# Performance work log

Measured on AMD Instinct MI355X. Metric: run time of the kernel, lower is better.

Reference implementation:

```python
import jax, jax.numpy as jnp
import numpy as np

B, C, H, W = 8, 512, 64, 64
CDIV = 8
CFG = C // CDIV  # f/g channels = 64


def setup_inputs() -> dict:
    key = jax.random.key(0)
    ks = jax.random.split(key, 8)
    x = jax.random.normal(ks[0], (B, C, H, W), dtype=jnp.float32)
    # 1x1 conv weights (spectral-norm omitted: weights used as-given), orthogonal-ish small init
    Wf = jax.random.normal(ks[1], (CFG, C), dtype=jnp.float32) * 0.02
    bf = jnp.zeros((CFG,), dtype=jnp.float32)
    Wg = jax.random.normal(ks[2], (CFG, C), dtype=jnp.float32) * 0.02
    bg = jnp.zeros((CFG,), dtype=jnp.float32)
    Wh = jax.random.normal(ks[3], (C, C), dtype=jnp.float32) * 0.02
    bh = jnp.zeros((C,), dtype=jnp.float32)
    # module inits gamma=0 (identity output); use 0.5 so the attention path is exercised
    gamma = jnp.float32(0.5)
    return {"x": x, "Wf": Wf, "bf": bf, "Wg": Wg, "bg": bg, "Wh": Wh, "bh": bh, "gamma": gamma}


def reference(x, Wf, bf, Wg, bg, Wh, bh, gamma):
    Bb, Cc, Hh, Ww = x.shape
    N = Hh * Ww
    xf = x.reshape(Bb, Cc, N)  # [B, C, N]
    # 1x1 convs == per-pixel linear maps
    f = jnp.einsum('oc,bcn->bon', Wf, xf) + bf[:, None]  # [B, CFG, N]
    g = jnp.einsum('oc,bcn->bon', Wg, xf) + bg[:, None]  # [B, CFG, N]
    h = jnp.einsum('oc,bcn->bon', Wh, xf) + bh[:, None]  # [B, C, N]
    # attention scores over spatial tokens: queries g, keys f -> [B, N, N]
    s = jnp.einsum('bci,bcj->bij', g, f)
    beta = jax.nn.softmax(s, axis=-1)
    o = jnp.einsum('bij,bcj->bci', beta, h).reshape(Bb, Cc, Hh, Ww)
    return gamma * o + x
```

## Files before the change

kernel.cpp:

```cpp
#include <hip/hip_runtime.h>
#include <hip/hip_bf16.h>

typedef __bf16 bf16;
typedef __attribute__((ext_vector_type(2))) __bf16 bf16x2;
typedef __attribute__((ext_vector_type(4))) __bf16 bf16x4;
typedef __attribute__((ext_vector_type(8))) __bf16 bf16x8;
typedef __attribute__((ext_vector_type(4))) float f32x4;
typedef __attribute__((ext_vector_type(4))) int i32x4;
typedef __attribute__((ext_vector_type(8))) int i32x8;
typedef unsigned char u8;

#define MFMA16x16x32 __builtin_amdgcn_mfma_f32_16x16x32_bf16
#define MFMA_MX(a, b, c, sa, sb) \
    __builtin_amdgcn_mfma_scale_f32_16x16x128_f8f6f4((a), (b), (c), 0, 0, 0, (sa), 0, (sb))

#define CAT8(lo, hi) (i32x8){(lo)[0], (lo)[1], (lo)[2], (lo)[3], (hi)[0], (hi)[1], (hi)[2], (hi)[3]}

#define NB 8
#define NC 512
#define NN 4096
#define CFG 64

#define XP 520
#define TP 74

#define EXP_OFF 4.5f
#define SCALE_ONE 0x7F7F7F7F

__global__ __launch_bounds__(256) void k_wprep(
    const float* __restrict__ Wf, const float* __restrict__ bfv,
    const float* __restrict__ Wg, const float* __restrict__ bgv,
    const float* __restrict__ Wh,
    bf16* __restrict__ Wfg, bf16* __restrict__ Whb, float* __restrict__ bfg)
{
    int idx = blockIdx.x * 256 + threadIdx.x;
    if (idx < 32768)       Wfg[idx] = (bf16)Wf[idx];
    else if (idx < 65536)  Wfg[idx] = (bf16)Wg[idx - 32768];
    if (idx < 262144)      Whb[idx] = (bf16)Wh[idx];
    if (idx < 64)          bfg[idx] = bfv[idx];
    else if (idx < 128)    bfg[idx] = bgv[idx - 64];
}

__global__ __launch_bounds__(512) void k_fused(
    const float* __restrict__ x, const bf16* __restrict__ Wfg,
    const float* __restrict__ bfg, const bf16* __restrict__ Whb,
    const float* __restrict__ bh,
    bf16* __restrict__ fF, bf16* __restrict__ gF, u8* __restrict__ hT)
{
    __shared__ bf16 X[64 * XP];
    __shared__ bf16 tile[64 * TP];

    int b = blockIdx.x, n0 = blockIdx.y * 64;
    int t = threadIdx.x;

    for (int cc = 0; cc < 8; cc++) {
        int cl = t >> 3, seg = (t & 7) * 8;
        const float* src = x + ((size_t)(b * NC + cc * 64 + cl)) * NN + n0 + seg;
        float4 v0 = ((const float4*)src)[0];
        float4 v1 = ((const float4*)src)[1];
        bf16* tr = &tile[cl * TP + seg];
        *(bf16x2*)(tr + 0) = bf16x2{(bf16)v0.x, (bf16)v0.y};
        *(bf16x2*)(tr + 2) = bf16x2{(bf16)v0.z, (bf16)v0.w};
        *(bf16x2*)(tr + 4) = bf16x2{(bf16)v1.x, (bf16)v1.y};
        *(bf16x2*)(tr + 6) = bf16x2{(bf16)v1.z, (bf16)v1.w};
        __syncthreads();
        int nl = t >> 3, cs = (t & 7) * 8;
        bf16 buf[8];
#pragma unroll
        for (int u = 0; u < 8; u++) buf[u] = tile[(cs + u) * TP + nl];
        *(bf16x8*)&X[nl * XP + cc * 64 + cs] = *(bf16x8*)buf;
        __syncthreads();
    }

    int w = t >> 6, l = t & 63;
    int lr = l & 15, lq = l >> 4;

    {
        const bf16* Ab = Whb + (size_t)(w * 64) * NC;
        f32x4 acc[4][4] = {};
        for (int k0 = 0; k0 < NC; k0 += 32) {
            bf16x8 a[4], bb[4];
#pragma unroll
            for (int fi = 0; fi < 4; fi++)
                a[fi] = *(const bf16x8*)(Ab + (size_t)(fi*16 + lr) * NC + k0 + lq*8);
#pragma unroll
            for (int fj = 0; fj < 4; fj++)
                bb[fj] = *(const bf16x8*)&X[(fj*16 + lr) * XP + k0 + lq*8];
#pragma unroll
            for (int fi = 0; fi < 4; fi++)
#pragma unroll
                for (int fj = 0; fj < 4; fj++)
                    acc[fi][fj] = MFMA16x16x32(bb[fj], a[fi], acc[fi][fj], 0, 0, 0);
        }
#pragma unroll
        for (int fi = 0; fi < 4; fi++) {
            int c = w*64 + fi*16 + lr;
            float bias = bh[c];
            size_t ctile = (size_t)(c >> 4);
#pragma unroll
            for (int fj = 0; fj < 4; fj++) {
                int j0 = n0 + fj*16 + lq*4;
                float v0 = acc[fi][fj][0] + bias;
                float v1 = acc[fi][fj][1] + bias;
                float v2 = acc[fi][fj][2] + bias;
                float v3 = acc[fi][fj][3] + bias;
                int pk = __builtin_amdgcn_cvt_pk_fp8_f32(v0, v1, 0, false);
                pk     = __builtin_amdgcn_cvt_pk_fp8_f32(v2, v3, pk, true);
                size_t tile128 = (size_t)(b*32) + (size_t)(j0 >> 7);
                size_t hk   = (size_t)((j0 >> 4) & 1);
                size_t lane = (size_t)(((j0 >> 5) & 3)*16 + (c & 15));
                size_t off = ((tile128*32 + ctile)*2 + hk)*1024 + lane*16 + (size_t)(j0 & 15);
                *(int*)(hT + off) = pk;
            }
        }
    }

    {
        const bf16* Bb = Wfg + (size_t)(w * 16) * NC;
        f32x4 acc2[4] = {};
        for (int k0 = 0; k0 < NC; k0 += 32) {
            bf16x8 a[4], bo;
#pragma unroll
            for (int fi = 0; fi < 4; fi++)
                a[fi] = *(const bf16x8*)&X[(fi*16 + lr) * XP + k0 + lq*8];
            bo = *(const bf16x8*)(Bb + (size_t)lr * NC + k0 + lq*8);
#pragma unroll
            for (int fi = 0; fi < 4; fi++)
                acc2[fi] = MFMA16x16x32(a[fi], bo, acc2[fi], 0, 0, 0);
        }
#pragma unroll
        for (int fi = 0; fi < 4; fi++)
#pragma unroll
            for (int tt = 0; tt < 4; tt++) {
                int n = n0 + fi*16 + lq*4 + tt;
                int o = w*16 + lr;
                float v = acc2[fi][tt] + bfg[o];
                int c = o & 63;
                bf16* dst = (o < 64) ? fF : gF;
                int jt16 = n >> 4, nr = n & 15;
                int ks = c >> 5, lqd = (c >> 3) & 3, e = c & 7;
                size_t off = (((size_t)(b*256 + jt16)*2 + ks)*64 + (lqd*16 + nr))*8 + e;
                dst[off] = (bf16)v;
            }
    }
}

__global__ __launch_bounds__(1024, 4) void k_attn(
    const bf16* __restrict__ fF, const bf16* __restrict__ gF,
    const u8* __restrict__ hT, const float* __restrict__ x,
    const float* __restrict__ gammap, float* __restrict__ out)
{
    __shared__ alignas(16) u8 Pl[2][16384];
    __shared__ alignas(16) bf16 fS[2][8192];
    __shared__ float lpart[8][2][16];
    __shared__ alignas(16) float linv[128];

    int b  = blockIdx.x;
    int i0 = blockIdx.y * 128;
    int t = threadIdx.x;
    int w = t >> 6, l = t & 63;
    int lr = l & 15, lq = l >> 4;

    float gamma = *gammap;
    int fi_s = w >> 1;
    int ks_s = w & 1;
    const int sone = SCALE_ONE;

    u8* Pf = &Pl[0][0];

    const bf16* gbase = gF + ((size_t)(b*256 + (i0 >> 4) + fi_s)*2)*512 + (size_t)l*8;
    bf16x8 bg0 = *(const bf16x8*)(gbase);
    bf16x8 bg1 = *(const bf16x8*)(gbase + 512);

    const bf16* fb0 = fF + (size_t)b*256*2*512;
    const u8* hb0 = hT + (size_t)b*2097152 + (size_t)(w*2)*2048 + (size_t)l*16;

    f32x4 oacc[8][2] = {};
    float lsum = 0.f;

#define F_LOAD(q, reg)  { (reg) = *(const bf16x8*)(fb0 + (size_t)(q)*8192 + t*8); }
#define F_WRITE(q, reg) { *(bf16x8*)&fS[(q) & 1][t*8] = (reg); }

#define S_STEP(jn, fbuf, pbuf)                                                 \
    {                                                                          \
        const bf16* fb = &fS[fbuf][((jn) & 1)*4096 + ks_s*2048] + l*8;         \
        bf16x8 af00 = *(const bf16x8*)(fb);                                    \
        bf16x8 af01 = *(const bf16x8*)(fb + 512);                              \
        bf16x8 af10 = *(const bf16x8*)(fb + 1024);                             \
        bf16x8 af11 = *(const bf16x8*)(fb + 1536);                             \
        f32x4 s0 = {}, s1 = {};                                                \
        s0 = MFMA16x16x32(af00, bg0, s0, 0, 0, 0);                             \
        s0 = MFMA16x16x32(af01, bg1, s0, 0, 0, 0);                             \
        s1 = MFMA16x16x32(af10, bg0, s1, 0, 0, 0);                             \
        s1 = MFMA16x16x32(af11, bg1, s1, 0, 0, 0);                             \
        float e00 = __expf(s0[0] - EXP_OFF), e01 = __expf(s0[1] - EXP_OFF);    \
        float e02 = __expf(s0[2] - EXP_OFF), e03 = __expf(s0[3] - EXP_OFF);    \
        float e10 = __expf(s1[0] - EXP_OFF), e11 = __expf(s1[1] - EXP_OFF);    \
        float e12 = __expf(s1[2] - EXP_OFF), e13 = __expf(s1[3] - EXP_OFF);    \
        lsum += (e00 + e01 + e02 + e03) + (e10 + e11 + e12 + e13);             \
        int pk0 = __builtin_amdgcn_cvt_pk_fp8_f32(e00, e01, 0, false);         \
        pk0     = __builtin_amdgcn_cvt_pk_fp8_f32(e02, e03, pk0, true);        \
        int pk1 = __builtin_amdgcn_cvt_pk_fp8_f32(e10, e11, 0, false);         \
        pk1     = __builtin_amdgcn_cvt_pk_fp8_f32(e12, e13, pk1, true);        \
        u8* pw = Pf + (pbuf)*16384 + fi_s*2048                                 \
                 + ((((jn) & 1)*2 + ks_s)*16 + lr)*16 + lq*4;                  \
        *(int*)(pw)        = pk0;                                              \
        *(int*)(pw + 1024) = pk1;                                              \
    }

#define PV_STEP(ph, pbuf)                                                      \
    {                                                                          \
        const u8* hb = hb0 + (size_t)(ph)*65536;                               \
        i32x4 hl0 = *(const i32x4*)(hb);                                       \
        i32x4 hh0 = *(const i32x4*)(hb + 1024);                                \
        i32x4 hl1 = *(const i32x4*)(hb + 2048);                                \
        i32x4 hh1 = *(const i32x4*)(hb + 3072);                                \
        i32x8 ah0 = CAT8(hl0, hh0);                                            \
        i32x8 ah1 = CAT8(hl1, hh1);                                            \
        const u8* Pr = Pf + (pbuf)*16384 + l*16;                               \
        __builtin_amdgcn_s_setprio(1);                                         \
        _Pragma("unroll")                                                      \
        for (int fi = 0; fi < 8; fi++) {                                       \
            i32x4 plo = *(const i32x4*)(Pr + fi*2048);                         \
            i32x4 phi = *(const i32x4*)(Pr + fi*2048 + 1024);                  \
            i32x8 ap = CAT8(plo, phi);                                         \
            oacc[fi][0] = MFMA_MX(ap, ah0, oacc[fi][0], sone, sone);           \
            oacc[fi][1] = MFMA_MX(ap, ah1, oacc[fi][1], sone, sone);           \
        }                                                                      \
        __builtin_amdgcn_s_setprio(0);                                         \
    }

    {
        bf16x8 fr;
        F_LOAD(0, fr)
        F_WRITE(0, fr)
        __syncthreads();
        F_LOAD(1, fr)
        S_STEP(0, 0, 0)
        S_STEP(1, 0, 0)
        F_WRITE(1, fr)
        __syncthreads();
    }

    for (int p = 0; p < 30; p++) {
        int cur = p & 1, nxt = cur ^ 1;

        bf16x8 fr;
        F_LOAD(p + 2, fr)

        PV_STEP(p, cur)

        S_STEP(2*p + 2, nxt, nxt)
        S_STEP(2*p + 3, nxt, nxt)

        F_WRITE(p + 2, fr)

        __syncthreads();
    }

    PV_STEP(30, 0)
    S_STEP(62, 1, 1)
    S_STEP(63, 1, 1)
    __syncthreads();
    PV_STEP(31, 1)

#undef S_STEP
#undef PV_STEP
#undef F_LOAD
#undef F_WRITE

    lsum += __shfl_xor(lsum, 16, 64);
    lsum += __shfl_xor(lsum, 32, 64);
    if (lq == 0) lpart[fi_s][ks_s][lr] = lsum;
    __syncthreads();
    if (t < 128) {
        linv[t] = 1.0f / (lpart[t >> 4][0][t & 15] + lpart[t >> 4][1][t & 15]);
    }
    __syncthreads();

    int cw = w * 32;
    const float* xb = x + (size_t)b * NC * NN;
    float* ob = out + (size_t)b * NC * NN;
#pragma unroll
    for (int fi = 0; fi < 8; fi++) {
        f32x4 li = *(const f32x4*)&linv[fi*16 + lq*4];
#pragma unroll
        for (int fc = 0; fc < 2; fc++) {
            int c = cw + fc*16 + lr;
            size_t base = (size_t)c * NN + i0 + fi*16 + lq*4;
            float4 xv = *(const float4*)(xb + base);
            float4 ov;
            ov.x = gamma * oacc[fi][fc][0] * li[0] + xv.x;
            ov.y = gamma * oacc[fi][fc][1] * li[1] + xv.y;
            ov.z = gamma * oacc[fi][fc][2] * li[2] + xv.z;
            ov.w = gamma * oacc[fi][fc][3] * li[3] + xv.w;
            *(float4*)(ob + base) = ov;
        }
    }
}

extern "C" void kernel_launch(void* const* d_in, const int* in_sizes, int n_in,
                              void* d_out, int out_size, void* d_ws, size_t ws_size,
                              hipStream_t stream)
{
    const float* x     = (const float*)d_in[0];
    const float* Wf    = (const float*)d_in[1];
    const float* bf_   = (const float*)d_in[2];
    const float* Wg    = (const float*)d_in[3];
    const float* bg_   = (const float*)d_in[4];
    const float* Wh    = (const float*)d_in[5];
    const float* bh_   = (const float*)d_in[6];
    const float* gamma = (const float*)d_in[7];
    float* out = (float*)d_out;

    char* ws = (char*)d_ws;
    u8*    hT  = (u8*)(ws + 33554432);
    bf16*  fF  = (bf16*)(ws + 67108864);
    bf16*  gF  = (bf16*)(ws + 71303168);
    bf16*  Wfg = (bf16*)(ws + 75497472);
    bf16*  Whb = (bf16*)(ws + 75628544);
    float* bfg = (float*)(ws + 76152832);

    k_wprep<<<dim3(1024), dim3(256), 0, stream>>>(Wf, bf_, Wg, bg_, Wh, Wfg, Whb, bfg);
    k_fused<<<dim3(8, 64), dim3(512), 0, stream>>>(x, Wfg, bfg, Whb, bh_, fF, gF, hT);
    k_attn<<<dim3(8, 32), dim3(1024), 0, stream>>>(fF, gF, hT, x, gamma, out);
}
```

Measured before the change: 165.5 us.

## Shrink attention query tile to 64 rows with 8 waves per block

Halves the query tile per attention block from 128 to 64 rows and cuts the block from 16 to 8 waves. Each wave now covers 64 output channels instead of 32, so every P fragment read from LDS feeds four MFMAs instead of two. The grid doubles to 512 blocks, which gives more blocks to spread across CUs and shrinks the shared-memory footprint. In exchange, every key and value tile is loaded twice as often overall, raising global traffic for f and h.

```diff
diff --git a/kernel.cpp b/kernel.cpp
--- a/kernel.cpp
+++ b/kernel.cpp
@@ -145,18 +145,18 @@
     }
 }
 
-__global__ __launch_bounds__(1024, 4) void k_attn(
+__global__ __launch_bounds__(512, 4) void k_attn(
     const bf16* __restrict__ fF, const bf16* __restrict__ gF,
     const u8* __restrict__ hT, const float* __restrict__ x,
     const float* __restrict__ gammap, float* __restrict__ out)
 {
-    __shared__ alignas(16) u8 Pl[2][16384];
+    __shared__ alignas(16) u8 Pl[2][8192];
     __shared__ alignas(16) bf16 fS[2][8192];
-    __shared__ float lpart[8][2][16];
-    __shared__ alignas(16) float linv[128];
+    __shared__ float lpart[4][2][16];
+    __shared__ alignas(16) float linv[64];
 
     int b  = blockIdx.x;
-    int i0 = blockIdx.y * 128;
+    int i0 = blockIdx.y * 64;
     int t = threadIdx.x;
     int w = t >> 6, l = t & 63;
     int lr = l & 15, lq = l >> 4;
@@ -173,13 +173,21 @@
     bf16x8 bg1 = *(const bf16x8*)(gbase + 512);
 
     const bf16* fb0 = fF + (size_t)b*256*2*512;
-    const u8* hb0 = hT + (size_t)b*2097152 + (size_t)(w*2)*2048 + (size_t)l*16;
-
-    f32x4 oacc[8][2] = {};
+    const u8* hb0 = hT + (size_t)b*2097152 + (size_t)(w*4)*2048 + (size_t)l*16;
+
+    f32x4 oacc[4][4] = {};
     float lsum = 0.f;
 
-#define F_LOAD(q, reg)  { (reg) = *(const bf16x8*)(fb0 + (size_t)(q)*8192 + t*8); }
-#define F_WRITE(q, reg) { *(bf16x8*)&fS[(q) & 1][t*8] = (reg); }
+#define F_LOAD(q, r0, r1)                                                      \
+    {                                                                          \
+        (r0) = *(const bf16x8*)(fb0 + (size_t)(q)*8192 + t*8);                 \
+        (r1) = *(const bf16x8*)(fb0 + (size_t)(q)*8192 + 4096 + t*8);          \
+    }
+#define F_WRITE(q, r0, r1)                                                     \
+    {                                                                          \
+        *(bf16x8*)&fS[(q) & 1][t*8]        = (r0);                             \
+        *(bf16x8*)&fS[(q) & 1][4096 + t*8] = (r1);                             \
+    }
 
 #define S_STEP(jn, fbuf, pbuf)                                                 \
     {                                                                          \
@@ -202,7 +210,7 @@
         pk0     = __builtin_amdgcn_cvt_pk_fp8_f32(e02, e03, pk0, true);        \
         int pk1 = __builtin_amdgcn_cvt_pk_fp8_f32(e10, e11, 0, false);         \
         pk1     = __builtin_amdgcn_cvt_pk_fp8_f32(e12, e13, pk1, true);        \
-        u8* pw = Pf + (pbuf)*16384 + fi_s*2048                                 \
+        u8* pw = Pf + (pbuf)*8192 + fi_s*2048                                  \
                  + ((((jn) & 1)*2 + ks_s)*16 + lr)*16 + lq*4;                  \
         *(int*)(pw)        = pk0;                                              \
         *(int*)(pw + 1024) = pk1;                                              \
@@ -211,49 +219,51 @@
 #define PV_STEP(ph, pbuf)                                                      \
     {                                                                          \
         const u8* hb = hb0 + (size_t)(ph)*65536;                               \
-        i32x4 hl0 = *(const i32x4*)(hb);                                       \
-        i32x4 hh0 = *(const i32x4*)(hb + 1024);                                \
-        i32x4 hl1 = *(const i32x4*)(hb + 2048);                                \
-        i32x4 hh1 = *(const i32x4*)(hb + 3072);                                \
-        i32x8 ah0 = CAT8(hl0, hh0);                                            \
-        i32x8 ah1 = CAT8(hl1, hh1);                                            \
-        const u8* Pr = Pf + (pbuf)*16384 + l*16;                               \
+        i32x8 ah[4];                                                           \
+        _Pragma("unroll")                                                      \
+        for (int fc = 0; fc < 4; fc++) {                                       \
+            i32x4 hl = *(const i32x4*)(hb + fc*2048);                          \
+            i32x4 hh = *(const i32x4*)(hb + fc*2048 + 1024);                   \
+            ah[fc] = CAT8(hl, hh);                                             \
+        }                                                                      \
+        const u8* Pr = Pf + (pbuf)*8192 + l*16;                                \
         __builtin_amdgcn_s_setprio(1);                                         \
         _Pragma("unroll")                                                      \
-        for (int fi = 0; fi < 8; fi++) {                                       \
+        for (int fi = 0; fi < 4; fi++) {                                       \
             i32x4 plo = *(const i32x4*)(Pr + fi*2048);                         \
             i32x4 phi = *(const i32x4*)(Pr + fi*2048 + 1024);                  \
             i32x8 ap = CAT8(plo, phi);                                         \
-            oacc[fi][0] = MFMA_MX(ap, ah0, oacc[fi][0], sone, sone);           \
-            oacc[fi][1] = MFMA_MX(ap, ah1, oacc[fi][1], sone, sone);           \
+            _Pragma("unroll")                                                  \
+            for (int fc = 0; fc < 4; fc++)                                     \
+                oacc[fi][fc] = MFMA_MX(ap, ah[fc], oacc[fi][fc], sone, sone);  \
         }                                                                      \
         __builtin_amdgcn_s_setprio(0);                                         \
     }
 
     {
-        bf16x8 fr;
-        F_LOAD(0, fr)
-        F_WRITE(0, fr)
-        __syncthreads();
-        F_LOAD(1, fr)
+        bf16x8 fr0, fr1;
+        F_LOAD(0, fr0, fr1)
+        F_WRITE(0, fr0, fr1)
+        __syncthreads();
+        F_LOAD(1, fr0, fr1)
         S_STEP(0, 0, 0)
         S_STEP(1, 0, 0)
-        F_WRITE(1, fr)
+        F_WRITE(1, fr0, fr1)
         __syncthreads();
     }
 
     for (int p = 0; p < 30; p++) {
         int cur = p & 1, nxt = cur ^ 1;
 
-        bf16x8 fr;
-        F_LOAD(p + 2, fr)
+        bf16x8 fr0, fr1;
+        F_LOAD(p + 2, fr0, fr1)
 
         PV_STEP(p, cur)
 
         S_STEP(2*p + 2, nxt, nxt)
         S_STEP(2*p + 3, nxt, nxt)
 
-        F_WRITE(p + 2, fr)
+        F_WRITE(p + 2, fr0, fr1)
 
         __syncthreads();
     }
@@ -273,19 +283,19 @@
     lsum += __shfl_xor(lsum, 32, 64);
     if (lq == 0) lpart[fi_s][ks_s][lr] = lsum;
     __syncthreads();
-    if (t < 128) {
+    if (t < 64) {
         linv[t] = 1.0f / (lpart[t >> 4][0][t & 15] + lpart[t >> 4][1][t & 15]);
     }
     __syncthreads();
 
-    int cw = w * 32;
+    int cw = w * 64;
     const float* xb = x + (size_t)b * NC * NN;
     float* ob = out + (size_t)b * NC * NN;
 #pragma unroll
-    for (int fi = 0; fi < 8; fi++) {
+    for (int fi = 0; fi < 4; fi++) {
         f32x4 li = *(const f32x4*)&linv[fi*16 + lq*4];
 #pragma unroll
-        for (int fc = 0; fc < 2; fc++) {
+        for (int fc = 0; fc < 4; fc++) {
             int c = cw + fc*16 + lr;
             size_t base = (size_t)c * NN + i0 + fi*16 + lq*4;
             float4 xv = *(const float4*)(xb + base);
@@ -323,5 +333,5 @@
 
     k_wprep<<<dim3(1024), dim3(256), 0, stream>>>(Wf, bf_, Wg, bg_, Wh, Wfg, Whb, bfg);
     k_fused<<<dim3(8, 64), dim3(512), 0, stream>>>(x, Wfg, bfg, Whb, bh_, fF, gF, hT);
-    k_attn<<<dim3(8, 32), dim3(1024), 0, stream>>>(fF, gF, hT, x, gamma, out);
+    k_attn<<<dim3(8, 64), dim3(512), 0, stream>>>(fF, gF, hT, x, gamma, out);
 }
```

Measured after the change: 177.1 us. 1.07x slower.

## Split attention channels across two 512-thread blocks per query tile

Applied to the files above, without the earlier changes.

The attention kernel drops from 1024 to 512 threads per block, and each block now handles half of the 512 output channels for its 128-query tile, so twice as many blocks are launched. Each wave now computes the scores for both key-split halves on its own instead of sharing them with a partner wave. The aim is better occupancy and finer scheduling granularity. In exchange, the QK^T scores, exponentials and P writes are duplicated across the two channel-half blocks, which doubles the softmax and score work.

```diff
diff --git a/kernel.cpp b/kernel.cpp
--- a/kernel.cpp
+++ b/kernel.cpp
@@ -145,25 +145,25 @@
     }
 }
 
-__global__ __launch_bounds__(1024, 4) void k_attn(
+__global__ __launch_bounds__(512, 4) void k_attn(
     const bf16* __restrict__ fF, const bf16* __restrict__ gF,
     const u8* __restrict__ hT, const float* __restrict__ x,
     const float* __restrict__ gammap, float* __restrict__ out)
 {
     __shared__ alignas(16) u8 Pl[2][16384];
     __shared__ alignas(16) bf16 fS[2][8192];
-    __shared__ float lpart[8][2][16];
+    __shared__ float lpart[8][16];
     __shared__ alignas(16) float linv[128];
 
     int b  = blockIdx.x;
-    int i0 = blockIdx.y * 128;
+    int i0 = (blockIdx.y >> 1) * 128;
+    int ch = blockIdx.y & 1;
     int t = threadIdx.x;
     int w = t >> 6, l = t & 63;
     int lr = l & 15, lq = l >> 4;
 
     float gamma = *gammap;
-    int fi_s = w >> 1;
-    int ks_s = w & 1;
+    int fi_s = w;
     const int sone = SCALE_ONE;
 
     u8* Pf = &Pl[0][0];
@@ -173,17 +173,25 @@
     bf16x8 bg1 = *(const bf16x8*)(gbase + 512);
 
     const bf16* fb0 = fF + (size_t)b*256*2*512;
-    const u8* hb0 = hT + (size_t)b*2097152 + (size_t)(w*2)*2048 + (size_t)l*16;
+    const u8* hb0 = hT + (size_t)b*2097152 + (size_t)(ch*16 + w*2)*2048 + (size_t)l*16;
 
     f32x4 oacc[8][2] = {};
     float lsum = 0.f;
 
-#define F_LOAD(q, reg)  { (reg) = *(const bf16x8*)(fb0 + (size_t)(q)*8192 + t*8); }
-#define F_WRITE(q, reg) { *(bf16x8*)&fS[(q) & 1][t*8] = (reg); }
-
-#define S_STEP(jn, fbuf, pbuf)                                                 \
+#define F_LOAD(q, r0, r1)                                                      \
     {                                                                          \
-        const bf16* fb = &fS[fbuf][((jn) & 1)*4096 + ks_s*2048] + l*8;         \
+        (r0) = *(const bf16x8*)(fb0 + (size_t)(q)*8192 + t*8);                 \
+        (r1) = *(const bf16x8*)(fb0 + (size_t)(q)*8192 + 4096 + t*8);          \
+    }
+#define F_WRITE(q, r0, r1)                                                     \
+    {                                                                          \
+        *(bf16x8*)&fS[(q) & 1][t*8]        = (r0);                             \
+        *(bf16x8*)&fS[(q) & 1][4096 + t*8] = (r1);                             \
+    }
+
+#define S_STEP(jn, ks, fbuf, pbuf)                                             \
+    {                                                                          \
+        const bf16* fb = &fS[fbuf][((jn) & 1)*4096 + (ks)*2048] + l*8;         \
         bf16x8 af00 = *(const bf16x8*)(fb);                                    \
         bf16x8 af01 = *(const bf16x8*)(fb + 512);                              \
         bf16x8 af10 = *(const bf16x8*)(fb + 1024);                             \
@@ -203,7 +211,7 @@
         int pk1 = __builtin_amdgcn_cvt_pk_fp8_f32(e10, e11, 0, false);         \
         pk1     = __builtin_amdgcn_cvt_pk_fp8_f32(e12, e13, pk1, true);        \
         u8* pw = Pf + (pbuf)*16384 + fi_s*2048                                 \
-                 + ((((jn) & 1)*2 + ks_s)*16 + lr)*16 + lq*4;                  \
+                 + ((((jn) & 1)*2 + (ks))*16 + lr)*16 + lq*4;                  \
         *(int*)(pw)        = pk0;                                              \
         *(int*)(pw + 1024) = pk1;                                              \
     }
@@ -231,36 +239,42 @@
     }
 
     {
-        bf16x8 fr;
-        F_LOAD(0, fr)
-        F_WRITE(0, fr)
-        __syncthreads();
-        F_LOAD(1, fr)
-        S_STEP(0, 0, 0)
-        S_STEP(1, 0, 0)
-        F_WRITE(1, fr)
+        bf16x8 fr0, fr1;
+        F_LOAD(0, fr0, fr1)
+        F_WRITE(0, fr0, fr1)
+        __syncthreads();
+        F_LOAD(1, fr0, fr1)
+        S_STEP(0, 0, 0, 0)
+        S_STEP(0, 1, 0, 0)
+        S_STEP(1, 0, 0, 0)
+        S_STEP(1, 1, 0, 0)
+        F_WRITE(1, fr0, fr1)
         __syncthreads();
     }
 
     for (int p = 0; p < 30; p++) {
         int cur = p & 1, nxt = cur ^ 1;
 
-        bf16x8 fr;
-        F_LOAD(p + 2, fr)
+        bf16x8 fr0, fr1;
+        F_LOAD(p + 2, fr0, fr1)
 
         PV_STEP(p, cur)
 
-        S_STEP(2*p + 2, nxt, nxt)
-        S_STEP(2*p + 3, nxt, nxt)
-
-        F_WRITE(p + 2, fr)
+        S_STEP(2*p + 2, 0, nxt, nxt)
+        S_STEP(2*p + 2, 1, nxt, nxt)
+        S_STEP(2*p + 3, 0, nxt, nxt)
+        S_STEP(2*p + 3, 1, nxt, nxt)
+
+        F_WRITE(p + 2, fr0, fr1)
 
         __syncthreads();
     }
 
     PV_STEP(30, 0)
-    S_STEP(62, 1, 1)
-    S_STEP(63, 1, 1)
+    S_STEP(62, 0, 1, 1)
+    S_STEP(62, 1, 1, 1)
+    S_STEP(63, 0, 1, 1)
+    S_STEP(63, 1, 1, 1)
     __syncthreads();
     PV_STEP(31, 1)
 
@@ -271,14 +285,14 @@
 
     lsum += __shfl_xor(lsum, 16, 64);
     lsum += __shfl_xor(lsum, 32, 64);
-    if (lq == 0) lpart[fi_s][ks_s][lr] = lsum;
+    if (lq == 0) lpart[w][lr] = lsum;
     __syncthreads();
     if (t < 128) {
-        linv[t] = 1.0f / (lpart[t >> 4][0][t & 15] + lpart[t >> 4][1][t & 15]);
+        linv[t] = 1.0f / lpart[t >> 4][t & 15];
     }
     __syncthreads();
 
-    int cw = w * 32;
+    int cw = ch*256 + w*32;
     const float* xb = x + (size_t)b * NC * NN;
     float* ob = out + (size_t)b * NC * NN;
 #pragma unroll
@@ -323,5 +337,5 @@
 
     k_wprep<<<dim3(1024), dim3(256), 0, stream>>>(Wf, bf_, Wg, bg_, Wh, Wfg, Whb, bfg);
     k_fused<<<dim3(8, 64), dim3(512), 0, stream>>>(x, Wfg, bfg, Whb, bh_, fF, gF, hT);
-    k_attn<<<dim3(8, 32), dim3(1024), 0, stream>>>(fF, gF, hT, x, gamma, out);
+    k_attn<<<dim3(8, 64), dim3(512), 0, stream>>>(fF, gF, hT, x, gamma, out);
 }
```

Result: slower. 190.6 us (+15.2%).
